# Kernel optimization log

Hardware: AMD Instinct MI355X
Metric: run time of the kernel (lower is better)

## Reference

```python
import jax, jax.numpy as jnp
import numpy as np

N_HEADS = 16

def _rope_tables(L, head_dim, dtype):
    inv_freq = 1.0 / (10000.0 ** (jnp.arange(0, head_dim, 2, dtype=jnp.float32) / head_dim))
    t = jnp.arange(L, dtype=jnp.float32)
    freqs = jnp.outer(t, inv_freq)            # [L, head_dim/2]
    emb = jnp.concatenate([freqs, freqs], -1)  # [L, head_dim]
    return jnp.cos(emb).astype(dtype), jnp.sin(emb).astype(dtype)

def _apply_rope(x, cos, sin):
    # x: [B, L, H, hd]; cos/sin: [1, L, 1, hd]
    half = x.shape[-1] // 2
    x1, x2 = x[..., :half], x[..., half:]
    x_rot = jnp.concatenate([-x2, x1], -1)
    return x * cos + x_rot * sin

def setup_inputs() -> dict:
    key = jax.random.key(0)
    ks = jax.random.split(key, 5)
    D = 1024
    s = 0.02
    return {
        "x": jax.random.normal(ks[0], (4, 2048, D), jnp.float32),
        "w_qkv": jax.random.normal(ks[1], (3 * D, D), jnp.float32) * s,
        "b_qkv": jax.random.normal(ks[2], (3 * D,), jnp.float32) * s,
        "w_out": jax.random.normal(ks[3], (D, D), jnp.float32) * s,
        "b_out": jax.random.normal(ks[4], (D,), jnp.float32) * s,
    }

def reference(x, w_qkv, b_qkv, w_out, b_out):
    B, L, D = x.shape
    H = N_HEADS
    hd = D // H
    scale = hd ** -0.5
    qkv = (x @ w_qkv.T + b_qkv).reshape(B, L, 3, H, hd)
    q, k, v = qkv[:, :, 0], qkv[:, :, 1], qkv[:, :, 2]  # [B,L,H,hd]
    cos, sin = _rope_tables(L, hd, x.dtype)
    cos = cos[None, :, None, :]
    sin = sin[None, :, None, :]
    q = _apply_rope(q, cos, sin)
    k = _apply_rope(k, cos, sin)
    # [B,H,L,L] scores, non-causal softmax
    attn = jnp.einsum('blhd,bmhd->bhlm', q, k) * scale
    attn = jax.nn.softmax(attn, axis=-1)
    out = jnp.einsum('bhlm,bmhd->blhd', attn, v).reshape(B, L, D)
    return out @ w_out.T + b_out
```

## Files before the change

### kernel.cpp

```cpp
#include <hip/hip_runtime.h>
#include <stdint.h>

typedef __attribute__((ext_vector_type(4))) float f32x4;
typedef __attribute__((ext_vector_type(8))) short bf16x8;
typedef __attribute__((ext_vector_type(4))) short s16x4;
typedef __attribute__((ext_vector_type(4))) float fp32x4;

#define QSCALE 0.18033688f

__device__ __forceinline__ short f2bf(float f) {
    union { float f; unsigned u; } v; v.f = f;
    unsigned u = v.u;
    unsigned r = u + 0x7fffu + ((u >> 16) & 1u);
    return (short)(r >> 16);
}
__device__ __forceinline__ unsigned cvtpk(float a, float b) {
    unsigned r;
    asm("v_cvt_pk_bf16_f32 %0, %1, %2" : "=v"(r) : "v"(a), "v"(b));
    return r;
}

__device__ __forceinline__ void gld_lds16(const void* g, void* l) {
    __builtin_amdgcn_global_load_lds(
        (const __attribute__((address_space(1))) unsigned int*)(uintptr_t)g,
        (__attribute__((address_space(3))) unsigned int*)(uintptr_t)l,
        16, 0, 0);
}

__global__ __launch_bounds__(256) void prep_kernel(const float* __restrict__ x,
                                                   const float* __restrict__ wq,
                                                   const float* __restrict__ wo,
                                                   short* __restrict__ xb,
                                                   short* __restrict__ wqb,
                                                   short* __restrict__ wob,
                                                   float* __restrict__ tab) {
    int bid = blockIdx.x, tid = threadIdx.x;
    if (bid < 6144) {
        const float* in; short* out; int base;
        if (bid < 4096)      { in = x;  out = xb;  base = bid; }
        else if (bid < 5632) { in = wq; out = wqb; base = bid - 4096; }
        else                 { in = wo; out = wob; base = bid - 5632; }
        int idx = (base * 256 + tid) * 8;
        fp32x4 a = *(const fp32x4*)&in[idx];
        fp32x4 b = *(const fp32x4*)&in[idx + 4];
        union { unsigned w[4]; bf16x8 v; } u;
        u.w[0] = cvtpk(a[0], a[1]); u.w[1] = cvtpk(a[2], a[3]);
        u.w[2] = cvtpk(b[0], b[1]); u.w[3] = cvtpk(b[2], b[3]);
        *(bf16x8*)&out[idx] = u.v;
    } else {
        int idx = (bid - 6144) * 256 + tid;
        int l = idx >> 5, d = idx & 31;
        float inv = expf(-(float)d / 32.f * logf(10000.f));
        float ang = (float)l * inv;
        tab[idx * 2 + 0] = cosf(ang);
        tab[idx * 2 + 1] = sinf(ang);
    }
}

template<int MODE>
__global__ __launch_bounds__(256, 2)
void gemm_bt(const short* __restrict__ A,
             const short* __restrict__ B,
             const float* __restrict__ bias,
             void* __restrict__ Cout,
             short* __restrict__ VTout,
             const float* __restrict__ tab,
             int M, int N, int K) {
    __shared__ short lds[2 * 16384];
    const int tid = threadIdx.x;
    const int lane = tid & 63, wave = tid >> 6;
    const int i15 = lane & 15, g = lane >> 4;
    const int wr = wave >> 1, wc = wave & 1;

    const int nbx = gridDim.x;
    int bid = blockIdx.y * nbx + blockIdx.x;
    const int xcd = bid & 7, idx = bid >> 3;
    const int nchunk = nbx >> 3;
    const int n0 = (xcd * nchunk + (idx % nchunk)) * 128;
    const int m0 = (idx / nchunk) * 128;

    const int xr3 = i15 & 3, xb2 = (i15 >> 2) & 1;
    const int cLo = g ^ xr3;
    const int aoff0 = (wr * 64 + i15) * 64 + (xb2 * 4 + cLo) * 8;
    const int aoff1 = (wr * 64 + i15) * 64 + ((1 ^ xb2) * 4 + cLo) * 8;
    const int boff0 = (wc * 64 + i15) * 64 + (xb2 * 4 + cLo) * 8;
    const int boff1 = (wc * 64 + i15) * 64 + ((1 ^ xb2) * 4 + cLo) * 8;

    const int srow = tid >> 3;
    const int ss = (tid & 7) ^ (srow & 7);
    const short* a0 = A + (size_t)(m0 + srow) * K + ss * 8;
    const short* a1 = a0 + (size_t)32 * K;
    const short* a2 = a0 + (size_t)64 * K;
    const short* a3 = a0 + (size_t)96 * K;
    const short* b0 = B + (size_t)(n0 + srow) * K + ss * 8;
    const short* b1 = b0 + (size_t)32 * K;
    const short* b2 = b0 + (size_t)64 * K;
    const short* b3 = b0 + (size_t)96 * K;

#define STAGE(slot)                                                       \
    do {                                                                  \
        gld_lds16(a0, lds + (slot) * 16384 + 0 * 2048 + wave * 512);      \
        gld_lds16(a1, lds + (slot) * 16384 + 1 * 2048 + wave * 512);      \
        gld_lds16(a2, lds + (slot) * 16384 + 2 * 2048 + wave * 512);      \
        gld_lds16(a3, lds + (slot) * 16384 + 3 * 2048 + wave * 512);      \
        gld_lds16(b0, lds + (slot) * 16384 + 8192 + 0 * 2048 + wave * 512); \
        gld_lds16(b1, lds + (slot) * 16384 + 8192 + 1 * 2048 + wave * 512); \
        gld_lds16(b2, lds + (slot) * 16384 + 8192 + 2 * 2048 + wave * 512); \
        gld_lds16(b3, lds + (slot) * 16384 + 8192 + 3 * 2048 + wave * 512); \
        a0 += 64; a1 += 64; a2 += 64; a3 += 64;                           \
        b0 += 64; b1 += 64; b2 += 64; b3 += 64;                           \
    } while (0)

    STAGE(0);

    f32x4 acc[4][4] = {};
    const int NT = K >> 6;

    for (int T = 0; T < NT; ++T) {
        const int cur = T & 1;
        if (T > 0) {
            __builtin_amdgcn_s_barrier();
            __builtin_amdgcn_sched_barrier(0);
        }
        if (T + 1 < NT) {
            STAGE(cur ^ 1);
            asm volatile("s_waitcnt vmcnt(8)" ::: "memory");
        } else {
            asm volatile("s_waitcnt vmcnt(0)" ::: "memory");
        }
        __builtin_amdgcn_s_barrier();
        __builtin_amdgcn_sched_barrier(0);

        const short* As_ = lds + cur * 16384;
        const short* Bs_ = As_ + 8192;
        bf16x8 af[4][2], bfr[4][2];
#pragma unroll
        for (int m = 0; m < 4; ++m) {
            af[m][0] = *(const bf16x8*)&As_[aoff0 + m * 1024];
            af[m][1] = *(const bf16x8*)&As_[aoff1 + m * 1024];
        }
#pragma unroll
        for (int n = 0; n < 4; ++n) {
            bfr[n][0] = *(const bf16x8*)&Bs_[boff0 + n * 1024];
            bfr[n][1] = *(const bf16x8*)&Bs_[boff1 + n * 1024];
        }
        __builtin_amdgcn_s_setprio(1);
#pragma unroll
        for (int m = 0; m < 4; ++m)
#pragma unroll
            for (int n = 0; n < 4; ++n)
#pragma unroll
                for (int ks = 0; ks < 2; ++ks)
                    acc[m][n] = __builtin_amdgcn_mfma_f32_16x16x32_bf16(af[m][ks], bfr[n][ks], acc[m][n], 0, 0, 0);
        __builtin_amdgcn_s_setprio(0);
    }
#undef STAGE

    if (MODE == 0) {
#pragma unroll
        for (int m = 0; m < 4; ++m)
#pragma unroll
            for (int n = 0; n < 4; ++n) {
                int col = n0 + wc * 64 + n * 16 + i15;
                float bcol = bias[col];
#pragma unroll
                for (int j = 0; j < 4; ++j) {
                    int row = m0 + wr * 64 + m * 16 + g * 4 + j;
                    ((float*)Cout)[(size_t)row * N + col] = acc[m][n][j] + bcol;
                }
            }
    } else {
        const int sec = n0 >> 10;
        if (sec < 2) {
            const float qs = (sec == 0) ? QSCALE : 1.0f;
            short* out = (short*)Cout;
#pragma unroll
            for (int m = 0; m < 4; ++m) {
#pragma unroll
                for (int pp = 0; pp < 2; ++pp) {
                    int d = pp * 16 + i15;
                    int collo = n0 + wc * 64 + pp * 16 + i15;
                    float blo = bias[collo], bhi = bias[collo + 32];
#pragma unroll
                    for (int j = 0; j < 4; ++j) {
                        int row = m0 + wr * 64 + m * 16 + g * 4 + j;
                        int l = row & 2047;
                        float2 cs = *(const float2*)&tab[(l * 32 + d) * 2];
                        float x1 = acc[m][pp][j] + blo;
                        float x2 = acc[m][pp + 2][j] + bhi;
                        out[(size_t)row * 3072 + collo]      = f2bf((x1 * cs.x - x2 * cs.y) * qs);
                        out[(size_t)row * 3072 + collo + 32] = f2bf((x2 * cs.x + x1 * cs.y) * qs);
                    }
                }
            }
        } else {
#pragma unroll
            for (int m = 0; m < 4; ++m) {
                int rbase = m0 + wr * 64 + m * 16 + g * 4;
                int lbase = rbase & 2047, bidx = rbase >> 11;
#pragma unroll
                for (int n = 0; n < 4; ++n) {
                    int vcol = (n0 - 2048) + wc * 64 + n * 16 + i15;
                    int h = vcol >> 6, d = vcol & 63;
                    float bb = bias[n0 + wc * 64 + n * 16 + i15];
                    union { unsigned w[2]; s16x4 v; } u;
                    u.w[0] = cvtpk(acc[m][n][0] + bb, acc[m][n][1] + bb);
                    u.w[1] = cvtpk(acc[m][n][2] + bb, acc[m][n][3] + bb);
                    *(s16x4*)&VTout[((size_t)(bidx * 16 + h) * 64 + d) * 2048 + lbase] = u.v;
                }
            }
        }
    }
}

__global__ __launch_bounds__(256, 4) void attn_kernel(const short* __restrict__ qkv,
                                                      const short* __restrict__ VT,
                                                      short* __restrict__ O) {
    __shared__ short Ks[2][64 * 64];
    __shared__ short Vs[2][64 * 64];
    int orig = blockIdx.x;
    int xcd = orig & 7, idx = orig >> 3;
    int bh = xcd * 8 + (idx >> 4), qt = idx & 15;
    int b = bh >> 4, h = bh & 15;
    int tid = threadIdx.x, lane = tid & 63, wave = tid >> 6;
    int i15 = lane & 15, g = lane >> 4;
    int q0 = qt * 128;

    size_t qbase = (size_t)(b * 2048 + q0 + wave * 32);
    bf16x8 qf[2][2];
#pragma unroll
    for (int qg = 0; qg < 2; ++qg) {
        qf[qg][0] = *(const bf16x8*)&qkv[(qbase + qg * 16 + i15) * 3072 + h * 64 + 0  + g * 8];
        qf[qg][1] = *(const bf16x8*)&qkv[(qbase + qg * 16 + i15) * 3072 + h * 64 + 32 + g * 8];
    }

    bf16x8 onesf;
#pragma unroll
    for (int e = 0; e < 8; ++e) onesf[e] = (short)0x3F80;

    const int srow = tid >> 3;
    const int ss8 = (tid & 7) ^ (srow & 7);
    const int pr0 = (srow & 0x23) | ((srow & 0x10) >> 2) | ((srow & 0x0C) << 1);
    const int sr1 = srow + 32;
    const int pr1 = (sr1 & 0x23) | ((sr1 & 0x10) >> 2) | ((sr1 & 0x0C) << 1);
    const short* kb_ = qkv + (size_t)(b * 2048) * 3072 + 1024 + h * 64 + ss8 * 8;
    const short* kp0 = kb_ + (size_t)pr0 * 3072;
    const short* kp1 = kb_ + (size_t)pr1 * 3072;
    const short* vb_ = VT + (size_t)bh * 64 * 2048 + ss8 * 8;
    const short* vp0 = vb_ + (size_t)srow * 2048;
    const short* vp1 = vb_ + (size_t)sr1 * 2048;

    const int xr3 = i15 & 3, xb2 = (i15 >> 2) & 1;
    const int cLo = g ^ xr3;
    const int o0 = i15 * 64 + (xb2 * 4 + cLo) * 8;
    const int o1 = i15 * 64 + ((1 ^ xb2) * 4 + cLo) * 8;

    f32x4 acc_o[2][4] = {};
    f32x4 acc_l[2] = {};

#define STAGE(bk, bv)                                        \
    do {                                                     \
        gld_lds16(kp0, (bk) + wave * 512);                   \
        gld_lds16(kp1, (bk) + 2048 + wave * 512);            \
        gld_lds16(vp0, (bv) + wave * 512);                   \
        gld_lds16(vp1, (bv) + 2048 + wave * 512);            \
        kp0 += (size_t)64 * 3072; kp1 += (size_t)64 * 3072;  \
        vp0 += 64; vp1 += 64;                                \
    } while (0)

    STAGE(Ks[0], Vs[0]);

    for (int t = 0; t < 32; ++t) {
        const int cur = t & 1;
        if (t > 0) {
            __builtin_amdgcn_s_barrier();
            __builtin_amdgcn_sched_barrier(0);
        }
        if (t + 1 < 32) {
            STAGE(Ks[cur ^ 1], Vs[cur ^ 1]);
            asm volatile("s_waitcnt vmcnt(4)" ::: "memory");
        } else {
            asm volatile("s_waitcnt vmcnt(0)" ::: "memory");
        }
        __builtin_amdgcn_s_barrier();
        __builtin_amdgcn_sched_barrier(0);

        const short* ks = Ks[cur];
        const short* vs = Vs[cur];

        f32x4 sa[2][4] = {};
        __builtin_amdgcn_s_setprio(1);
#pragma unroll
        for (int kb = 0; kb < 2; ++kb) {
            const int ko = kb ? o1 : o0;
            bf16x8 kf[4];
#pragma unroll
            for (int jb = 0; jb < 4; ++jb) kf[jb] = *(const bf16x8*)&ks[ko + jb * 1024];
#pragma unroll
            for (int qg = 0; qg < 2; ++qg)
#pragma unroll
                for (int jb = 0; jb < 4; ++jb)
                    sa[qg][jb] = __builtin_amdgcn_mfma_f32_16x16x32_bf16(kf[jb], qf[qg][kb], sa[qg][jb], 0, 0, 0);
        }
        __builtin_amdgcn_s_setprio(0);

        bf16x8 pf[2][2];
#pragma unroll
        for (int qg = 0; qg < 2; ++qg) {
            float p[4][4];
#pragma unroll
            for (int jb = 0; jb < 4; ++jb)
#pragma unroll
                for (int r = 0; r < 4; ++r)
                    p[jb][r] = __builtin_amdgcn_exp2f(sa[qg][jb][r]);
#pragma unroll
            for (int kb = 0; kb < 2; ++kb) {
                union { unsigned w[4]; bf16x8 v; } u;
                u.w[0] = cvtpk(p[2 * kb][0],     p[2 * kb][1]);
                u.w[1] = cvtpk(p[2 * kb][2],     p[2 * kb][3]);
                u.w[2] = cvtpk(p[2 * kb + 1][0], p[2 * kb + 1][1]);
                u.w[3] = cvtpk(p[2 * kb + 1][2], p[2 * kb + 1][3]);
                pf[qg][kb] = u.v;
            }
        }

        __builtin_amdgcn_s_setprio(1);
#pragma unroll
        for (int db = 0; db < 4; ++db) {
#pragma unroll
            for (int kb = 0; kb < 2; ++kb) {
                bf16x8 vf = *(const bf16x8*)&vs[(kb ? o1 : o0) + db * 1024];
#pragma unroll
                for (int qg = 0; qg < 2; ++qg)
                    acc_o[qg][db] = __builtin_amdgcn_mfma_f32_16x16x32_bf16(pf[qg][kb], vf, acc_o[qg][db], 0, 0, 0);
            }
        }
#pragma unroll
        for (int qg = 0; qg < 2; ++qg) {
            acc_l[qg] = __builtin_amdgcn_mfma_f32_16x16x32_bf16(pf[qg][0], onesf, acc_l[qg], 0, 0, 0);
            acc_l[qg] = __builtin_amdgcn_mfma_f32_16x16x32_bf16(pf[qg][1], onesf, acc_l[qg], 0, 0, 0);
        }
        __builtin_amdgcn_s_setprio(0);
    }
#undef STAGE

#pragma unroll
    for (int qg = 0; qg < 2; ++qg) {
        float linv4[4];
#pragma unroll
        for (int r = 0; r < 4; ++r) linv4[r] = 1.f / acc_l[qg][r];
#pragma unroll
        for (int db = 0; db < 4; ++db) {
            int ocol = h * 64 + db * 16 + i15;
#pragma unroll
            for (int r = 0; r < 4; ++r) {
                size_t orow = qbase + qg * 16 + g * 4 + r;
                O[orow * 1024 + ocol] = f2bf(acc_o[qg][db][r] * linv4[r]);
            }
        }
    }
}

extern "C" void kernel_launch(void* const* d_in, const int* in_sizes, int n_in,
                              void* d_out, int out_size, void* d_ws, size_t ws_size,
                              hipStream_t stream) {
    const float* x     = (const float*)d_in[0];
    const float* w_qkv = (const float*)d_in[1];
    const float* b_qkv = (const float*)d_in[2];
    const float* w_out = (const float*)d_in[3];
    const float* b_out = (const float*)d_in[4];

    char* ws = (char*)d_ws;
    short* qkvb = (short*)(ws);
    short* xb   = (short*)(ws + 50331648);
    short* wqb  = (short*)(ws + 67108864);
    short* wob  = (short*)(ws + 73400320);
    short* VT   = (short*)(ws + 75497472);
    float* rt   = (float*)(ws + 92274688);
    short* Ob   = xb;

    prep_kernel<<<6400, 256, 0, stream>>>(x, w_qkv, w_out, xb, wqb, wob, rt);

    gemm_bt<1><<<dim3(24, 64), 256, 0, stream>>>(xb, wqb, b_qkv, qkvb, VT, rt, 8192, 3072, 1024);
    attn_kernel<<<1024, 256, 0, stream>>>(qkvb, VT, Ob);
    gemm_bt<0><<<dim3(8, 64), 256, 0, stream>>>(Ob, wob, b_out, d_out, nullptr, nullptr, 8192, 1024, 1024);
}
```

Before: 167.5 us.

## Halve GEMM K-tile to 32 and raise occupancy to four blocks per CU

Shrinks the per-stage K tile in the bf16 GEMM from 64 to 32, halving shared memory to 32 KB, and raises the launch-bounds occupancy hint from 2 to 4 blocks per CU. Staging, the LDS swizzle and the fragment loads are rewritten for the narrower 32-wide rows. The aim is more resident waves to hide global-load latency. In exchange there are twice as many barrier-synchronised iterations with half the MFMA work each, and a tighter register budget that may cause spills.

```diff
diff --git a/kernel.cpp b/kernel.cpp
--- a/kernel.cpp
+++ b/kernel.cpp
@@ -58,7 +58,7 @@
 }
 
 template<int MODE>
-__global__ __launch_bounds__(256, 2)
+__global__ __launch_bounds__(256, 4)
 void gemm_bt(const short* __restrict__ A,
              const short* __restrict__ B,
              const float* __restrict__ bias,
@@ -66,7 +66,7 @@
              short* __restrict__ VTout,
              const float* __restrict__ tab,
              int M, int N, int K) {
-    __shared__ short lds[2 * 16384];
+    __shared__ short lds[2 * 8192];
     const int tid = threadIdx.x;
     const int lane = tid & 63, wave = tid >> 6;
     const int i15 = lane & 15, g = lane >> 4;
@@ -79,42 +79,30 @@
     const int n0 = (xcd * nchunk + (idx % nchunk)) * 128;
     const int m0 = (idx / nchunk) * 128;
 
-    const int xr3 = i15 & 3, xb2 = (i15 >> 2) & 1;
-    const int cLo = g ^ xr3;
-    const int aoff0 = (wr * 64 + i15) * 64 + (xb2 * 4 + cLo) * 8;
-    const int aoff1 = (wr * 64 + i15) * 64 + ((1 ^ xb2) * 4 + cLo) * 8;
-    const int boff0 = (wc * 64 + i15) * 64 + (xb2 * 4 + cLo) * 8;
-    const int boff1 = (wc * 64 + i15) * 64 + ((1 ^ xb2) * 4 + cLo) * 8;
-
-    const int srow = tid >> 3;
-    const int ss = (tid & 7) ^ (srow & 7);
-    const short* a0 = A + (size_t)(m0 + srow) * K + ss * 8;
-    const short* a1 = a0 + (size_t)32 * K;
-    const short* a2 = a0 + (size_t)64 * K;
-    const short* a3 = a0 + (size_t)96 * K;
-    const short* b0 = B + (size_t)(n0 + srow) * K + ss * 8;
-    const short* b1 = b0 + (size_t)32 * K;
-    const short* b2 = b0 + (size_t)64 * K;
-    const short* b3 = b0 + (size_t)96 * K;
-
-#define STAGE(slot)                                                       \
-    do {                                                                  \
-        gld_lds16(a0, lds + (slot) * 16384 + 0 * 2048 + wave * 512);      \
-        gld_lds16(a1, lds + (slot) * 16384 + 1 * 2048 + wave * 512);      \
-        gld_lds16(a2, lds + (slot) * 16384 + 2 * 2048 + wave * 512);      \
-        gld_lds16(a3, lds + (slot) * 16384 + 3 * 2048 + wave * 512);      \
-        gld_lds16(b0, lds + (slot) * 16384 + 8192 + 0 * 2048 + wave * 512); \
-        gld_lds16(b1, lds + (slot) * 16384 + 8192 + 1 * 2048 + wave * 512); \
-        gld_lds16(b2, lds + (slot) * 16384 + 8192 + 2 * 2048 + wave * 512); \
-        gld_lds16(b3, lds + (slot) * 16384 + 8192 + 3 * 2048 + wave * 512); \
-        a0 += 64; a1 += 64; a2 += 64; a3 += 64;                           \
-        b0 += 64; b1 += 64; b2 += 64; b3 += 64;                           \
+    const int csw = (g ^ (i15 & 3)) * 8;
+    const int aoff = (wr * 64 + i15) * 32 + csw;
+    const int boff = (wc * 64 + i15) * 32 + csw;
+
+    const int sr = lane >> 2;
+    const int sc = ((lane & 3) ^ (sr & 3)) * 8;
+    const short* a0 = A + (size_t)(m0 + (0 * 4 + wave) * 16 + sr) * K + sc;
+    const short* a1 = A + (size_t)(m0 + (1 * 4 + wave) * 16 + sr) * K + sc;
+    const short* b0 = B + (size_t)(n0 + (0 * 4 + wave) * 16 + sr) * K + sc;
+    const short* b1 = B + (size_t)(n0 + (1 * 4 + wave) * 16 + sr) * K + sc;
+
+#define STAGE(slot)                                                  \
+    do {                                                             \
+        gld_lds16(a0, lds + (slot) * 8192 + (0 * 4 + wave) * 512);   \
+        gld_lds16(a1, lds + (slot) * 8192 + (1 * 4 + wave) * 512);   \
+        gld_lds16(b0, lds + (slot) * 8192 + 4096 + (0 * 4 + wave) * 512); \
+        gld_lds16(b1, lds + (slot) * 8192 + 4096 + (1 * 4 + wave) * 512); \
+        a0 += 32; a1 += 32; b0 += 32; b1 += 32;                      \
     } while (0)
 
     STAGE(0);
 
     f32x4 acc[4][4] = {};
-    const int NT = K >> 6;
+    const int NT = K >> 5;
 
     for (int T = 0; T < NT; ++T) {
         const int cur = T & 1;
@@ -124,34 +112,26 @@
         }
         if (T + 1 < NT) {
             STAGE(cur ^ 1);
-            asm volatile("s_waitcnt vmcnt(8)" ::: "memory");
+            asm volatile("s_waitcnt vmcnt(4)" ::: "memory");
         } else {
             asm volatile("s_waitcnt vmcnt(0)" ::: "memory");
         }
         __builtin_amdgcn_s_barrier();
         __builtin_amdgcn_sched_barrier(0);
 
-        const short* As_ = lds + cur * 16384;
-        const short* Bs_ = As_ + 8192;
-        bf16x8 af[4][2], bfr[4][2];
-#pragma unroll
-        for (int m = 0; m < 4; ++m) {
-            af[m][0] = *(const bf16x8*)&As_[aoff0 + m * 1024];
-            af[m][1] = *(const bf16x8*)&As_[aoff1 + m * 1024];
-        }
-#pragma unroll
-        for (int n = 0; n < 4; ++n) {
-            bfr[n][0] = *(const bf16x8*)&Bs_[boff0 + n * 1024];
-            bfr[n][1] = *(const bf16x8*)&Bs_[boff1 + n * 1024];
-        }
+        const short* As_ = lds + cur * 8192;
+        const short* Bs_ = As_ + 4096;
+        bf16x8 af[4], bfr[4];
+#pragma unroll
+        for (int m = 0; m < 4; ++m) af[m] = *(const bf16x8*)&As_[aoff + m * 512];
+#pragma unroll
+        for (int n = 0; n < 4; ++n) bfr[n] = *(const bf16x8*)&Bs_[boff + n * 512];
         __builtin_amdgcn_s_setprio(1);
 #pragma unroll
         for (int m = 0; m < 4; ++m)
 #pragma unroll
             for (int n = 0; n < 4; ++n)
-#pragma unroll
-                for (int ks = 0; ks < 2; ++ks)
-                    acc[m][n] = __builtin_amdgcn_mfma_f32_16x16x32_bf16(af[m][ks], bfr[n][ks], acc[m][n], 0, 0, 0);
+                acc[m][n] = __builtin_amdgcn_mfma_f32_16x16x32_bf16(af[m], bfr[n], acc[m][n], 0, 0, 0);
         __builtin_amdgcn_s_setprio(0);
     }
 #undef STAGE
```

Measured after the change: 174.6 us. 4.3% more time.

## Load A fragments directly from global into registers, stage only B in LDS

Applied to the files above, without the earlier changes.

The GEMM stops staging the A tile through LDS. Each wave now loads its own A fragments straight from global memory into registers, and only B stays double-buffered in LDS, which halves LDS usage and drops the occupancy hint from the launch bounds. This removes the LDS write/read traffic for A, but the global loads are less coalesced (16-byte reads per lane across many rows). They are also duplicated across the two wc waves and are not covered by the prefetch pipeline, so latency may be exposed.

```diff
diff --git a/kernel.cpp b/kernel.cpp
--- a/kernel.cpp
+++ b/kernel.cpp
@@ -58,7 +58,7 @@
 }
 
 template<int MODE>
-__global__ __launch_bounds__(256, 2)
+__global__ __launch_bounds__(256)
 void gemm_bt(const short* __restrict__ A,
              const short* __restrict__ B,
              const float* __restrict__ bias,
@@ -66,7 +66,7 @@
              short* __restrict__ VTout,
              const float* __restrict__ tab,
              int M, int N, int K) {
-    __shared__ short lds[2 * 16384];
+    __shared__ short lds[2 * 8192];
     const int tid = threadIdx.x;
     const int lane = tid & 63, wave = tid >> 6;
     const int i15 = lane & 15, g = lane >> 4;
@@ -81,37 +81,31 @@
 
     const int xr3 = i15 & 3, xb2 = (i15 >> 2) & 1;
     const int cLo = g ^ xr3;
-    const int aoff0 = (wr * 64 + i15) * 64 + (xb2 * 4 + cLo) * 8;
-    const int aoff1 = (wr * 64 + i15) * 64 + ((1 ^ xb2) * 4 + cLo) * 8;
     const int boff0 = (wc * 64 + i15) * 64 + (xb2 * 4 + cLo) * 8;
     const int boff1 = (wc * 64 + i15) * 64 + ((1 ^ xb2) * 4 + cLo) * 8;
 
     const int srow = tid >> 3;
     const int ss = (tid & 7) ^ (srow & 7);
-    const short* a0 = A + (size_t)(m0 + srow) * K + ss * 8;
-    const short* a1 = a0 + (size_t)32 * K;
-    const short* a2 = a0 + (size_t)64 * K;
-    const short* a3 = a0 + (size_t)96 * K;
     const short* b0 = B + (size_t)(n0 + srow) * K + ss * 8;
     const short* b1 = b0 + (size_t)32 * K;
     const short* b2 = b0 + (size_t)64 * K;
     const short* b3 = b0 + (size_t)96 * K;
 
-#define STAGE(slot)                                                       \
-    do {                                                                  \
-        gld_lds16(a0, lds + (slot) * 16384 + 0 * 2048 + wave * 512);      \
-        gld_lds16(a1, lds + (slot) * 16384 + 1 * 2048 + wave * 512);      \
-        gld_lds16(a2, lds + (slot) * 16384 + 2 * 2048 + wave * 512);      \
-        gld_lds16(a3, lds + (slot) * 16384 + 3 * 2048 + wave * 512);      \
-        gld_lds16(b0, lds + (slot) * 16384 + 8192 + 0 * 2048 + wave * 512); \
-        gld_lds16(b1, lds + (slot) * 16384 + 8192 + 1 * 2048 + wave * 512); \
-        gld_lds16(b2, lds + (slot) * 16384 + 8192 + 2 * 2048 + wave * 512); \
-        gld_lds16(b3, lds + (slot) * 16384 + 8192 + 3 * 2048 + wave * 512); \
-        a0 += 64; a1 += 64; a2 += 64; a3 += 64;                           \
-        b0 += 64; b1 += 64; b2 += 64; b3 += 64;                           \
+    const short* aP0 = A + (size_t)(m0 + wr * 64 + 0 * 16 + i15) * K + g * 8;
+    const short* aP1 = A + (size_t)(m0 + wr * 64 + 1 * 16 + i15) * K + g * 8;
+    const short* aP2 = A + (size_t)(m0 + wr * 64 + 2 * 16 + i15) * K + g * 8;
+    const short* aP3 = A + (size_t)(m0 + wr * 64 + 3 * 16 + i15) * K + g * 8;
+
+#define STAGE_B(slot)                                                 \
+    do {                                                              \
+        gld_lds16(b0, lds + (slot) * 8192 + 0 * 2048 + wave * 512);   \
+        gld_lds16(b1, lds + (slot) * 8192 + 1 * 2048 + wave * 512);   \
+        gld_lds16(b2, lds + (slot) * 8192 + 2 * 2048 + wave * 512);   \
+        gld_lds16(b3, lds + (slot) * 8192 + 3 * 2048 + wave * 512);   \
+        b0 += 64; b1 += 64; b2 += 64; b3 += 64;                       \
     } while (0)
 
-    STAGE(0);
+    STAGE_B(0);
 
     f32x4 acc[4][4] = {};
     const int NT = K >> 6;
@@ -122,23 +116,25 @@
             __builtin_amdgcn_s_barrier();
             __builtin_amdgcn_sched_barrier(0);
         }
+        bf16x8 af[4][2];
+        af[0][0] = *(const bf16x8*)aP0; af[0][1] = *(const bf16x8*)(aP0 + 32);
+        af[1][0] = *(const bf16x8*)aP1; af[1][1] = *(const bf16x8*)(aP1 + 32);
+        af[2][0] = *(const bf16x8*)aP2; af[2][1] = *(const bf16x8*)(aP2 + 32);
+        af[3][0] = *(const bf16x8*)aP3; af[3][1] = *(const bf16x8*)(aP3 + 32);
+        aP0 += 64; aP1 += 64; aP2 += 64; aP3 += 64;
+        __builtin_amdgcn_sched_barrier(0);
         if (T + 1 < NT) {
-            STAGE(cur ^ 1);
-            asm volatile("s_waitcnt vmcnt(8)" ::: "memory");
+            STAGE_B(cur ^ 1);
+            __builtin_amdgcn_sched_barrier(0);
+            asm volatile("s_waitcnt vmcnt(4)" ::: "memory");
         } else {
             asm volatile("s_waitcnt vmcnt(0)" ::: "memory");
         }
         __builtin_amdgcn_s_barrier();
         __builtin_amdgcn_sched_barrier(0);
 
-        const short* As_ = lds + cur * 16384;
-        const short* Bs_ = As_ + 8192;
-        bf16x8 af[4][2], bfr[4][2];
-#pragma unroll
-        for (int m = 0; m < 4; ++m) {
-            af[m][0] = *(const bf16x8*)&As_[aoff0 + m * 1024];
-            af[m][1] = *(const bf16x8*)&As_[aoff1 + m * 1024];
-        }
+        const short* Bs_ = lds + cur * 8192;
+        bf16x8 bfr[4][2];
 #pragma unroll
         for (int n = 0; n < 4; ++n) {
             bfr[n][0] = *(const bf16x8*)&Bs_[boff0 + n * 1024];
@@ -154,7 +150,7 @@
                     acc[m][n] = __builtin_amdgcn_mfma_f32_16x16x32_bf16(af[m][ks], bfr[n][ks], acc[m][n], 0, 0, 0);
         __builtin_amdgcn_s_setprio(0);
     }
-#undef STAGE
+#undef STAGE_B
 
     if (MODE == 0) {
 #pragma unroll
```

After: 234.0 us, median of 2. +39.7%, slower.
